# Performance work log

Measured on AMD Instinct MI355X. Metric: run time of the kernel, lower is better.

The kernel has to match this reference:

```python
import jax, jax.numpy as jnp
import numpy as np

N = 100000   # nodes
E = 1600000  # edges (avg degree 16)
D = 64       # embedding_dim
H = 64       # hidden_dim


def setup_inputs() -> dict:
    key = jax.random.key(0)
    k = jax.random.split(key, 4)
    embedding = jax.random.normal(k[0], (N, D), dtype=jnp.float32)
    edge_index = jax.random.randint(k[1], (2, E), 0, N, dtype=jnp.int64)
    W1 = jax.random.normal(k[2], (D, H), dtype=jnp.float32) / np.sqrt(D).astype(np.float32)
    b1 = jnp.zeros((H,), jnp.float32)
    W2 = jax.random.normal(k[3], (H, D), dtype=jnp.float32) / np.sqrt(H).astype(np.float32)
    b2 = jnp.zeros((D,), jnp.float32)
    return {"embedding": embedding, "edge_index": edge_index,
            "W1": W1, "b1": b1, "W2": W2, "b2": b2}


def _gcn_layer(x, src, dst, norm, W, b, n):
    # linear transform first (small GEMM), then normalized scatter-add aggregation
    h = x @ W                                   # [n, out]
    msg = h[src] * norm[:, None]                # gather + scale, [E+n, out]
    out = jax.ops.segment_sum(msg, dst, num_segments=n)
    return out + b


def reference(embedding, edge_index, W1, b1, W2, b2):
    n = embedding.shape[0]
    loop = jnp.arange(n)
    # GCNConv adds self-loops before normalization
    src = jnp.concatenate([edge_index[0], loop])
    dst = jnp.concatenate([edge_index[1], loop])
    deg = jax.ops.segment_sum(jnp.ones_like(dst, dtype=embedding.dtype), dst, num_segments=n)
    dinv = jax.lax.rsqrt(deg)                   # deg >= 1 thanks to self-loops
    norm = dinv[src] * dinv[dst]                # symmetric D^-1/2 A_hat D^-1/2
    h1 = jax.nn.relu(_gcn_layer(embedding, src, dst, norm, W1, b1, n))
    h2 = jax.nn.relu(_gcn_layer(h1, src, dst, norm, W2, b2, n))
    return h2
```

## Files before the change

### kernel.cpp

```cpp
#include <hip/hip_runtime.h>
#include <hip/hip_fp16.h>


#define NBMAX 512
#define BCAP  5120
#define CHUNK 8192

__global__ __launch_bounds__(512) void bucket_scatter_kernel(
        const int* __restrict__ src, const int* __restrict__ dst,
        int* __restrict__ bucket_fill, unsigned int* __restrict__ bucketed,
        int E, int nb) {
    __shared__ int cnt[NBMAX];
    __shared__ int sc[NBMAX];
    __shared__ int exc[NBMAX + 1];
    __shared__ int rk[NBMAX];
    __shared__ int gb[NBMAX];
    __shared__ unsigned int pk[CHUNK];
    __shared__ unsigned short bid[CHUNK];
    int t = threadIdx.x;
    int base = blockIdx.x * CHUNK;
    cnt[t] = 0; rk[t] = 0;
    __syncthreads();
    unsigned int s[16]; int b[16];
#pragma unroll
    for (int j = 0; j < 16; ++j) {
        int e = base + j * 512 + t;
        if (e < E) {
            int d = dst[e];
            b[j] = d >> 8;
            s[j] = (unsigned int)src[e] | ((unsigned int)(d & 255) << 17);
            atomicAdd(&cnt[b[j]], 1);
        } else b[j] = -1;
    }
    __syncthreads();
    sc[t] = cnt[t];
    __syncthreads();
    for (int off = 1; off < NBMAX; off <<= 1) {
        int x = (t >= off) ? sc[t - off] : 0;
        __syncthreads();
        sc[t] += x;
        __syncthreads();
    }
    if (t == 0) exc[0] = 0;
    exc[t + 1] = sc[t];
    __syncthreads();
#pragma unroll
    for (int j = 0; j < 16; ++j) {
        if (b[j] >= 0) {
            int r = atomicAdd(&rk[b[j]], 1);
            int pos = exc[b[j]] + r;
            pk[pos] = s[j];
            bid[pos] = (unsigned short)b[j];
        }
    }
    if (t < nb && cnt[t] > 0) gb[t] = atomicAdd(&bucket_fill[t], cnt[t]);
    __syncthreads();
    int m = exc[NBMAX];
    for (int idx = t; idx < m; idx += 512) {
        int bb = bid[idx];
        int off = gb[bb] + (idx - exc[bb]);
        if (off < BCAP) bucketed[(size_t)bb * BCAP + off] = pk[idx];
    }
}

__global__ __launch_bounds__(256) void csr_build_kernel(
        const unsigned int* __restrict__ bucketed, const int* __restrict__ bucket_fill,
        int* __restrict__ row_ptr, float* __restrict__ dinv,
        int* __restrict__ col_src, int n, int nb) {
    __shared__ int bf[NBMAX];
    __shared__ int sc[NBMAX];
    __shared__ int cnt[256], rk2[256], sc2[256], lofs[256];
    __shared__ int cout[BCAP];
    int b = blockIdx.x, t = threadIdx.x;
    bf[t]       = (t < nb)       ? bucket_fill[t]       : 0;
    bf[t + 256] = (t + 256 < nb) ? bucket_fill[t + 256] : 0;
    __syncthreads();
    sc[t] = bf[t];
    sc[t + 256] = bf[t + 256];
    __syncthreads();
    for (int off = 1; off < NBMAX; off <<= 1) {
        int v0 = (t >= off) ? sc[t - off] : 0;
        int v1 = sc[t + 256 - off];
        __syncthreads();
        sc[t] += v0; sc[t + 256] += v1;
        __syncthreads();
    }
    cnt[t] = 0; rk2[t] = 0;
    __syncthreads();
    if (b == 0 && t == 0) row_ptr[n] = sc[nb - 1];
    int m = bf[b]; if (m > BCAP) m = BCAP;
    int gbase = sc[b] - bf[b];
    const unsigned int* ebase = bucketed + (size_t)b * BCAP;
    for (int i = t; i < m; i += 256)
        atomicAdd(&cnt[ebase[i] >> 17], 1);
    __syncthreads();
    int v = cnt[t];
    sc2[t] = v; __syncthreads();
    for (int off = 1; off < 256; off <<= 1) {
        int x = (t >= off) ? sc2[t - off] : 0;
        __syncthreads();
        sc2[t] += x;
        __syncthreads();
    }
    lofs[t] = sc2[t] - v;
    __syncthreads();
    int node = (b << 8) + t;
    if (node < n) {
        row_ptr[node] = gbase + lofs[t];
        dinv[node] = rsqrtf((float)(v + 1));
    }
    for (int i = t; i < m; i += 256) {
        unsigned int p = ebase[i];
        int dl = p >> 17;
        int r = atomicAdd(&rk2[dl], 1);
        cout[lofs[dl] + r] = (int)(p & 0x1FFFF);
    }
    __syncthreads();
    for (int i = t; i < m; i += 256) col_src[gbase + i] = cout[i];
}

__global__ __launch_bounds__(256, 4) void gemm_scale_kernel(
        const float* __restrict__ x, const float* __restrict__ W,
        const float* __restrict__ dinv, __half* __restrict__ g, int n) {
    __shared__ float4 ws4[64 * 16];
    int t = threadIdx.x;
    const float4* W4 = (const float4*)W;
#pragma unroll
    for (int j = 0; j < 4; ++j) ws4[j * 256 + t] = W4[j * 256 + t];
    __syncthreads();
    int cg = t & 7;
    int rg = t >> 3;
    int row0 = blockIdx.x * 128;
    const float4* x4 = (const float4*)x;
    int r[4];
#pragma unroll
    for (int j = 0; j < 4; ++j) {
        int rr = row0 + rg + 32 * j;
        r[j] = (rr < n) ? rr : 0;
    }
    float4 acc[4][2];
#pragma unroll
    for (int j = 0; j < 4; ++j) {
        acc[j][0] = make_float4(0.f, 0.f, 0.f, 0.f);
        acc[j][1] = make_float4(0.f, 0.f, 0.f, 0.f);
    }
#pragma unroll 2
    for (int kq = 0; kq < 16; ++kq) {
        float4 xv[4];
#pragma unroll
        for (int j = 0; j < 4; ++j) xv[j] = x4[(size_t)r[j] * 16 + kq];
#pragma unroll
        for (int kk = 0; kk < 4; ++kk) {
            int k = kq * 4 + kk;
            float4 w0 = ws4[k * 16 + 2 * cg];
            float4 w1 = ws4[k * 16 + 2 * cg + 1];
#pragma unroll
            for (int j = 0; j < 4; ++j) {
                float xk = ((const float*)&xv[j])[kk];
                acc[j][0].x = fmaf(xk, w0.x, acc[j][0].x);
                acc[j][0].y = fmaf(xk, w0.y, acc[j][0].y);
                acc[j][0].z = fmaf(xk, w0.z, acc[j][0].z);
                acc[j][0].w = fmaf(xk, w0.w, acc[j][0].w);
                acc[j][1].x = fmaf(xk, w1.x, acc[j][1].x);
                acc[j][1].y = fmaf(xk, w1.y, acc[j][1].y);
                acc[j][1].z = fmaf(xk, w1.z, acc[j][1].z);
                acc[j][1].w = fmaf(xk, w1.w, acc[j][1].w);
            }
        }
    }
    uint4* g16 = (uint4*)g;
#pragma unroll
    for (int j = 0; j < 4; ++j) {
        int rr = row0 + rg + 32 * j;
        if (rr < n) {
            float d = dinv[rr];
            __half2 h0 = __floats2half2_rn(acc[j][0].x * d, acc[j][0].y * d);
            __half2 h1 = __floats2half2_rn(acc[j][0].z * d, acc[j][0].w * d);
            __half2 h2 = __floats2half2_rn(acc[j][1].x * d, acc[j][1].y * d);
            __half2 h3 = __floats2half2_rn(acc[j][1].z * d, acc[j][1].w * d);
            uint4 u;
            u.x = *(unsigned int*)&h0;
            u.y = *(unsigned int*)&h1;
            u.z = *(unsigned int*)&h2;
            u.w = *(unsigned int*)&h3;
            g16[(size_t)rr * 8 + cg] = u;
        }
    }
}

__device__ __forceinline__ void acc_add_h8(float* acc, uint4 u) {
    const __half2* hp = (const __half2*)&u;
#pragma unroll
    for (int q = 0; q < 4; ++q) {
        float2 f = __half22float2(hp[q]);
        acc[2 * q]     += f.x;
        acc[2 * q + 1] += f.y;
    }
}

__global__ __launch_bounds__(256) void aggregate_kernel(
        const __half* __restrict__ g, const int* __restrict__ row_ptr,
        const int* __restrict__ col_src, const float* __restrict__ dinv,
        const float* __restrict__ bias, float* __restrict__ out, int n) {
    int wid = (blockIdx.x * 256 + threadIdx.x) >> 6;
    int lane = threadIdx.x & 63;
    int grp = lane >> 3;
    int l8  = lane & 7;
    if (wid >= n) return;
    const uint4* g16 = (const uint4*)g;
    float acc[8] = {0.f, 0.f, 0.f, 0.f, 0.f, 0.f, 0.f, 0.f};
    int beg = row_ptr[wid];
    int end = row_ptr[wid + 1];
    int i = beg + grp;
    for (; i + 8 < end; i += 16) {
        int s0 = col_src[i];
        int s1 = col_src[i + 8];
        uint4 u0 = g16[(size_t)s0 * 8 + l8];
        uint4 u1 = g16[(size_t)s1 * 8 + l8];
        const __half2* a = (const __half2*)&u0;
        const __half2* b = (const __half2*)&u1;
#pragma unroll
        for (int q = 0; q < 4; ++q) {
            __half2 sph = __hadd2(a[q], b[q]);
            float2 f = __half22float2(sph);
            acc[2 * q]     += f.x;
            acc[2 * q + 1] += f.y;
        }
    }
    for (; i < end; i += 8) {
        int s = col_src[i];
        uint4 u = g16[(size_t)s * 8 + l8];
        acc_add_h8(acc, u);
    }
#pragma unroll
    for (int c = 0; c < 8; ++c) {
        acc[c] += __shfl_xor(acc[c], 8, 64);
        acc[c] += __shfl_xor(acc[c], 16, 64);
        acc[c] += __shfl_xor(acc[c], 32, 64);
    }
    if (grp == 0) {
        uint4 us = g16[(size_t)wid * 8 + l8];
        acc_add_h8(acc, us);
        float d = dinv[wid];
        const float4* b4 = (const float4*)bias;
        float4 ba = b4[2 * l8], bb = b4[2 * l8 + 1];
        float4 o0, o1;
        o0.x = fmaxf(fmaf(acc[0], d, ba.x), 0.f);
        o0.y = fmaxf(fmaf(acc[1], d, ba.y), 0.f);
        o0.z = fmaxf(fmaf(acc[2], d, ba.z), 0.f);
        o0.w = fmaxf(fmaf(acc[3], d, ba.w), 0.f);
        o1.x = fmaxf(fmaf(acc[4], d, bb.x), 0.f);
        o1.y = fmaxf(fmaf(acc[5], d, bb.y), 0.f);
        o1.z = fmaxf(fmaf(acc[6], d, bb.z), 0.f);
        o1.w = fmaxf(fmaf(acc[7], d, bb.w), 0.f);
        float4* o4 = (float4*)out;
        o4[(size_t)wid * 16 + 2 * l8]     = o0;
        o4[(size_t)wid * 16 + 2 * l8 + 1] = o1;
    }
}

extern "C" void kernel_launch(void* const* d_in, const int* in_sizes, int n_in,
                              void* d_out, int out_size, void* d_ws, size_t ws_size,
                              hipStream_t stream) {
    const float* embedding = (const float*)d_in[0];
    const int*   edge_idx  = (const int*)d_in[1];
    const float* W1        = (const float*)d_in[2];
    const float* b1        = (const float*)d_in[3];
    const float* W2        = (const float*)d_in[4];
    const float* b2        = (const float*)d_in[5];
    float* out = (float*)d_out;

    const int n = in_sizes[0] / 64;
    const int E = in_sizes[1] / 2;
    const int* src = edge_idx;
    const int* dst = edge_idx + E;
    const int nb = (n + 255) >> 8;

    char* w = (char*)d_ws;
    auto alloc = [&](size_t bytes) {
        char* p = w;
        w += (bytes + 255) & ~(size_t)255;
        return p;
    };
    int*   row_ptr     = (int*)  alloc(((size_t)n + 1) * 4);
    float* dinv        = (float*)alloc((size_t)n * 4);
    int*   col_src     = (int*)  alloc((size_t)E * 4);
    int*   bucket_fill = (int*)  alloc((size_t)nb * 4);
    char*  gshare      = alloc((size_t)n * 64 * 4);
    __half* g          = (__half*)gshare;
    unsigned int* bucketed = (unsigned int*)gshare;

    hipMemsetAsync(bucket_fill, 0, (size_t)nb * 4, stream);
    bucket_scatter_kernel<<<(E + CHUNK - 1) / CHUNK, 512, 0, stream>>>(
        src, dst, bucket_fill, bucketed, E, nb);
    csr_build_kernel<<<nb, 256, 0, stream>>>(
        bucketed, bucket_fill, row_ptr, dinv, col_src, n, nb);

    const int gemm_blocks = (n + 127) / 128;
    const int agg_blocks  = (int)(((size_t)n * 64 + 255) / 256);

    gemm_scale_kernel<<<gemm_blocks, 256, 0, stream>>>(embedding, W1, dinv, g, n);
    aggregate_kernel<<<agg_blocks, 256, 0, stream>>>(g, row_ptr, col_src, dinv, b1, out, n);
    gemm_scale_kernel<<<gemm_blocks, 256, 0, stream>>>(out, W2, dinv, g, n);
    aggregate_kernel<<<agg_blocks, 256, 0, stream>>>(g, row_ptr, col_src, dinv, b2, out, n);
}
```

Baseline: 241.2 us.

## Reorder second GCN layer to aggregate before GEMM with fp16 intermediates

Layer 1's aggregate now writes relu(h1)*dinv in fp16 instead of fp32 output. Layer 2 aggregates that first and applies W2, bias and relu in a new GEMM kernel that reads fp16. This drops one fp32 write/read round trip of the hidden activations and puts the dinv scaling into the aggregate epilogue. The cost is an extra fp16 rounding of the aggregated layer-2 input before the GEMM, which may reduce accuracy.

Result: no change. 238.6 us (-1.1%).

```diff
diff --git a/kernel.cpp b/kernel.cpp
--- a/kernel.cpp
+++ b/kernel.cpp
@@ -119,7 +119,7 @@
     for (int i = t; i < m; i += 256) col_src[gbase + i] = cout[i];
 }
 
-__global__ __launch_bounds__(256, 4) void gemm_scale_kernel(
+__global__ __launch_bounds__(256, 4) void gemm_g_kernel(
         const float* __restrict__ x, const float* __restrict__ W,
         const float* __restrict__ dinv, __half* __restrict__ g, int n) {
     __shared__ float4 ws4[64 * 16];
@@ -198,10 +198,11 @@
     }
 }
 
+template<bool FUSE_MLP>
 __global__ __launch_bounds__(256) void aggregate_kernel(
         const __half* __restrict__ g, const int* __restrict__ row_ptr,
         const int* __restrict__ col_src, const float* __restrict__ dinv,
-        const float* __restrict__ bias, float* __restrict__ out, int n) {
+        const float* __restrict__ bias, __half* __restrict__ gout, int n) {
     int wid = (blockIdx.x * 256 + threadIdx.x) >> 6;
     int lane = threadIdx.x & 63;
     int grp = lane >> 3;
@@ -242,20 +243,108 @@
         uint4 us = g16[(size_t)wid * 8 + l8];
         acc_add_h8(acc, us);
         float d = dinv[wid];
-        const float4* b4 = (const float4*)bias;
-        float4 ba = b4[2 * l8], bb = b4[2 * l8 + 1];
-        float4 o0, o1;
-        o0.x = fmaxf(fmaf(acc[0], d, ba.x), 0.f);
-        o0.y = fmaxf(fmaf(acc[1], d, ba.y), 0.f);
-        o0.z = fmaxf(fmaf(acc[2], d, ba.z), 0.f);
-        o0.w = fmaxf(fmaf(acc[3], d, ba.w), 0.f);
-        o1.x = fmaxf(fmaf(acc[4], d, bb.x), 0.f);
-        o1.y = fmaxf(fmaf(acc[5], d, bb.y), 0.f);
-        o1.z = fmaxf(fmaf(acc[6], d, bb.z), 0.f);
-        o1.w = fmaxf(fmaf(acc[7], d, bb.w), 0.f);
-        float4* o4 = (float4*)out;
-        o4[(size_t)wid * 16 + 2 * l8]     = o0;
-        o4[(size_t)wid * 16 + 2 * l8 + 1] = o1;
+        float res[8];
+        if (FUSE_MLP) {
+            const float4* b4 = (const float4*)bias;
+            float4 ba = b4[2 * l8], bb = b4[2 * l8 + 1];
+            res[0] = fmaxf(fmaf(acc[0], d, ba.x), 0.f) * d;
+            res[1] = fmaxf(fmaf(acc[1], d, ba.y), 0.f) * d;
+            res[2] = fmaxf(fmaf(acc[2], d, ba.z), 0.f) * d;
+            res[3] = fmaxf(fmaf(acc[3], d, ba.w), 0.f) * d;
+            res[4] = fmaxf(fmaf(acc[4], d, bb.x), 0.f) * d;
+            res[5] = fmaxf(fmaf(acc[5], d, bb.y), 0.f) * d;
+            res[6] = fmaxf(fmaf(acc[6], d, bb.z), 0.f) * d;
+            res[7] = fmaxf(fmaf(acc[7], d, bb.w), 0.f) * d;
+        } else {
+#pragma unroll
+            for (int c = 0; c < 8; ++c) res[c] = acc[c] * d;
+        }
+        __half2 h0 = __floats2half2_rn(res[0], res[1]);
+        __half2 h1 = __floats2half2_rn(res[2], res[3]);
+        __half2 h2 = __floats2half2_rn(res[4], res[5]);
+        __half2 h3 = __floats2half2_rn(res[6], res[7]);
+        uint4 u;
+        u.x = *(unsigned int*)&h0;
+        u.y = *(unsigned int*)&h1;
+        u.z = *(unsigned int*)&h2;
+        u.w = *(unsigned int*)&h3;
+        ((uint4*)gout)[(size_t)wid * 8 + l8] = u;
+    }
+}
+
+__global__ __launch_bounds__(256, 4) void gemm_out_kernel(
+        const __half* __restrict__ xh, const float* __restrict__ W,
+        const float* __restrict__ bias, float* __restrict__ out, int n) {
+    __shared__ float4 ws4[64 * 16];
+    int t = threadIdx.x;
+    const float4* W4 = (const float4*)W;
+#pragma unroll
+    for (int j = 0; j < 4; ++j) ws4[j * 256 + t] = W4[j * 256 + t];
+    __syncthreads();
+    int cg = t & 7;
+    int rg = t >> 3;
+    int row0 = blockIdx.x * 128;
+    const uint2* x2 = (const uint2*)xh;
+    int r[4];
+#pragma unroll
+    for (int j = 0; j < 4; ++j) {
+        int rr = row0 + rg + 32 * j;
+        r[j] = (rr < n) ? rr : 0;
+    }
+    float4 acc[4][2];
+#pragma unroll
+    for (int j = 0; j < 4; ++j) {
+        acc[j][0] = make_float4(0.f, 0.f, 0.f, 0.f);
+        acc[j][1] = make_float4(0.f, 0.f, 0.f, 0.f);
+    }
+#pragma unroll 2
+    for (int kq = 0; kq < 16; ++kq) {
+        float xv[4][4];
+#pragma unroll
+        for (int j = 0; j < 4; ++j) {
+            uint2 u = x2[(size_t)r[j] * 16 + kq];
+            float2 fa = __half22float2(*(const __half2*)&u.x);
+            float2 fb = __half22float2(*(const __half2*)&u.y);
+            xv[j][0] = fa.x; xv[j][1] = fa.y; xv[j][2] = fb.x; xv[j][3] = fb.y;
+        }
+#pragma unroll
+        for (int kk = 0; kk < 4; ++kk) {
+            int k = kq * 4 + kk;
+            float4 w0 = ws4[k * 16 + 2 * cg];
+            float4 w1 = ws4[k * 16 + 2 * cg + 1];
+#pragma unroll
+            for (int j = 0; j < 4; ++j) {
+                float xk = xv[j][kk];
+                acc[j][0].x = fmaf(xk, w0.x, acc[j][0].x);
+                acc[j][0].y = fmaf(xk, w0.y, acc[j][0].y);
+                acc[j][0].z = fmaf(xk, w0.z, acc[j][0].z);
+                acc[j][0].w = fmaf(xk, w0.w, acc[j][0].w);
+                acc[j][1].x = fmaf(xk, w1.x, acc[j][1].x);
+                acc[j][1].y = fmaf(xk, w1.y, acc[j][1].y);
+                acc[j][1].z = fmaf(xk, w1.z, acc[j][1].z);
+                acc[j][1].w = fmaf(xk, w1.w, acc[j][1].w);
+            }
+        }
+    }
+    const float4* b4 = (const float4*)bias;
+    float4 bb0 = b4[2 * cg], bb1 = b4[2 * cg + 1];
+    float4* o4 = (float4*)out;
+#pragma unroll
+    for (int j = 0; j < 4; ++j) {
+        int rr = row0 + rg + 32 * j;
+        if (rr < n) {
+            float4 o0, o1;
+            o0.x = fmaxf(acc[j][0].x + bb0.x, 0.f);
+            o0.y = fmaxf(acc[j][0].y + bb0.y, 0.f);
+            o0.z = fmaxf(acc[j][0].z + bb0.z, 0.f);
+            o0.w = fmaxf(acc[j][0].w + bb0.w, 0.f);
+            o1.x = fmaxf(acc[j][1].x + bb1.x, 0.f);
+            o1.y = fmaxf(acc[j][1].y + bb1.y, 0.f);
+            o1.z = fmaxf(acc[j][1].z + bb1.z, 0.f);
+            o1.w = fmaxf(acc[j][1].w + bb1.w, 0.f);
+            o4[(size_t)rr * 16 + 2 * cg]     = o0;
+            o4[(size_t)rr * 16 + 2 * cg + 1] = o1;
+        }
     }
 }
 
@@ -286,9 +375,12 @@
     float* dinv        = (float*)alloc((size_t)n * 4);
     int*   col_src     = (int*)  alloc((size_t)E * 4);
     int*   bucket_fill = (int*)  alloc((size_t)nb * 4);
-    char*  gshare      = alloc((size_t)n * 64 * 4);
-    __half* g          = (__half*)gshare;
-    unsigned int* bucketed = (unsigned int*)gshare;
+    char*  regionA     = alloc((size_t)n * 64 * 2 > (size_t)nb * BCAP * 4
+                               ? (size_t)n * 64 * 2 : (size_t)nb * BCAP * 4);
+    unsigned int* bucketed = (unsigned int*)regionA;
+    __half* g1         = (__half*)regionA;
+    __half* a2         = g1;
+    __half* t1         = (__half*)alloc((size_t)n * 64 * 2);
 
     hipMemsetAsync(bucket_fill, 0, (size_t)nb * 4, stream);
     bucket_scatter_kernel<<<(E + CHUNK - 1) / CHUNK, 512, 0, stream>>>(
@@ -299,8 +391,10 @@
     const int gemm_blocks = (n + 127) / 128;
     const int agg_blocks  = (int)(((size_t)n * 64 + 255) / 256);
 
-    gemm_scale_kernel<<<gemm_blocks, 256, 0, stream>>>(embedding, W1, dinv, g, n);
-    aggregate_kernel<<<agg_blocks, 256, 0, stream>>>(g, row_ptr, col_src, dinv, b1, out, n);
-    gemm_scale_kernel<<<gemm_blocks, 256, 0, stream>>>(out, W2, dinv, g, n);
-    aggregate_kernel<<<agg_blocks, 256, 0, stream>>>(g, row_ptr, col_src, dinv, b2, out, n);
-}
+    gemm_g_kernel<<<gemm_blocks, 256, 0, stream>>>(embedding, W1, dinv, g1, n);
+    aggregate_kernel<true><<<agg_blocks, 256, 0, stream>>>(
+        g1, row_ptr, col_src, dinv, b1, t1, n);
+    aggregate_kernel<false><<<agg_blocks, 256, 0, stream>>>(
+        t1, row_ptr, col_src, dinv, b2 , a2, n);
+    gemm_out_kernel<<<gemm_blocks, 256, 0, stream>>>(a2, W2, b2, out, n);
+}
```
